# Kernel optimization log

Hardware: AMD Instinct MI355X
Metric: run time of the kernel (lower is better)

The kernel has to match this reference:

```python
import jax, jax.numpy as jnp
import numpy as np

H = 8          # num_heads
D = 64         # head_dim
HID = 512      # hidden_size
W = 128        # window_size
NEG = -1e9

def setup_inputs() -> dict:
    key = jax.random.key(0)
    ks = jax.random.split(key, 12)
    B, S = 2, 2048
    def lin(i):
        w = jax.random.normal(ks[i], (HID, HID), dtype=jnp.float32) * (1.0 / np.sqrt(HID))
        b = jax.random.normal(ks[i + 1], (HID,), dtype=jnp.float32) * 0.01
        return w, b
    Wq, bq = lin(0)
    Wk, bk = lin(2)
    Wv, bv = lin(4)
    Wo, bo = lin(6)
    return {
        "value": jax.random.normal(ks[8], (B, S, HID), dtype=jnp.float32),
        "key": jax.random.normal(ks[9], (B, S, HID), dtype=jnp.float32),
        "query": jax.random.normal(ks[10], (B, S, HID), dtype=jnp.float32),
        "Wq": Wq, "bq": bq, "Wk": Wk, "bk": bk,
        "Wv": Wv, "bv": bv, "Wo": Wo, "bo": bo,
    }

def reference(value, key, query, Wq, bq, Wk, bk, Wv, bv, Wo, bo):
    B, S, _ = query.shape
    def heads(x, Wt, b):
        # torch Linear: x @ W.T + b ; then [B,S,H,D] -> [B,H,S,D]
        return (x @ Wt.T + b).reshape(B, S, H, D).transpose(0, 2, 1, 3)
    Q = heads(query, Wq, bq)
    K = heads(key, Wk, bk)
    V = heads(value, Wv, bv)
    scores = jnp.einsum('bhqd,bhkd->bhqk', Q, K) / jnp.sqrt(jnp.float32(D))
    idx = jnp.arange(S)
    local = jnp.abs(idx[:, None] - idx[None, :]) <= W  # [S,S] band mask
    scores = jnp.where(local[None, None], scores, NEG)
    weights = jax.nn.softmax(scores, axis=-1)
    out = jnp.einsum('bhqk,bhkd->bhqd', weights, V)
    out = out.transpose(0, 2, 1, 3).reshape(B, S, HID)
    return out @ Wo.T + bo
```

## Files before the change

kernel.cpp:

```cpp
#include <hip/hip_runtime.h>
#include <stdint.h>

#define B_   2
#define S_   2048
#define H_   8
#define D_   64
#define HID_ 512
#define W_   128
#define M_   (B_ * S_)
#define E_   (M_ * HID_)
#define PPAD_ 72
#define M0_  12.0f

typedef unsigned short u16;
typedef __attribute__((ext_vector_type(8))) __bf16 bf16x8;
typedef __attribute__((ext_vector_type(4))) float  floatx4;

__device__ __forceinline__ float b2f(u16 u) {
    union { unsigned int i; float f; } x;
    x.i = ((unsigned int)u) << 16;
    return x.f;
}
__device__ __forceinline__ u16 f2b(float f) {
    union { float f; unsigned int i; } x;
    x.f = f;
    unsigned int r = x.i + 0x7FFFu + ((x.i >> 16) & 1u);
    return (u16)(r >> 16);
}

__device__ __forceinline__ void gll16(const u16* g, u16* l) {
    __builtin_amdgcn_global_load_lds(
        (const __attribute__((address_space(1))) unsigned int*)g,
        (__attribute__((address_space(3))) unsigned int*)l, 16, 0, 0);
}

__device__ __forceinline__ void cvt8_store(float4 a, float4 b, u16* dst) {
    bf16x8 v;
    v[0] = (__bf16)a.x; v[1] = (__bf16)a.y; v[2] = (__bf16)a.z; v[3] = (__bf16)a.w;
    v[4] = (__bf16)b.x; v[5] = (__bf16)b.y; v[6] = (__bf16)b.z; v[7] = (__bf16)b.w;
    *(bf16x8*)dst = v;
}

template <int MODE>
__device__ __forceinline__ void gemm_fp32in_body(
    const float* __restrict__ Xf, const float* __restrict__ Wf,
    const float* __restrict__ bias, u16* __restrict__ outH) {
    __shared__ u16 As[128 * 32];
    __shared__ u16 Bs[64 * 32];

    const int tid  = threadIdx.x;
    const int wave = tid >> 6;
    const int lane = tid & 63;
    const int r16  = lane & 15;
    const int quad = lane >> 4;
    const int m0 = blockIdx.x * 128;
    const int n0 = blockIdx.y * 64;
    const int m_base = m0 + wave * 64;

    const int ar = tid >> 2;
    const int ak = (tid & 3) * 8;
    const int br = tid >> 1;
    const int bk2 = (tid & 1) * 16;

    floatx4 zero = {0.f, 0.f, 0.f, 0.f};
    floatx4 acc[4][4];
#pragma unroll
    for (int i = 0; i < 4; i++)
#pragma unroll
        for (int j = 0; j < 4; j++) acc[i][j] = zero;

    for (int k0 = 0; k0 < HID_; k0 += 32) {
        __syncthreads();
#pragma unroll
        for (int e = 0; e < 4; e++) {
            const int row = e * 32 + ar;
            const float4* src = (const float4*)(Xf + (size_t)(m0 + row) * HID_ + k0 + ak);
            cvt8_store(src[0], src[1], &As[row * 32 + ak]);
        }
        {
            const float4* src = (const float4*)(Wf + (size_t)(n0 + br) * HID_ + k0 + bk2);
            cvt8_store(src[0], src[1], &Bs[br * 32 + bk2]);
            cvt8_store(src[2], src[3], &Bs[br * 32 + bk2 + 8]);
        }
        __syncthreads();

        bf16x8 a0[4], b[4];
#pragma unroll
        for (int t = 0; t < 4; t++) {
            a0[t] = *(const bf16x8*)&As[(wave * 64 + t * 16 + r16) * 32 + quad * 8];
            b[t]  = *(const bf16x8*)&Bs[(t * 16 + r16) * 32 + quad * 8];
        }
#pragma unroll
        for (int i = 0; i < 4; i++)
#pragma unroll
            for (int j = 0; j < 4; j++)
                acc[i][j] = __builtin_amdgcn_mfma_f32_16x16x32_bf16(a0[i], b[j], acc[i][j], 0, 0, 0);
    }

    const int bb = m_base >> 11;
    if (MODE == 1) {
#pragma unroll
        for (int j = 0; j < 4; j++) {
            const int col = n0 + j * 16 + r16;
            const int h = col >> 6, d = col & (D_ - 1);
            const float bv = bias[col];
            const size_t base = (size_t)(bb * H_ + h) * S_;
#pragma unroll
            for (int i = 0; i < 4; i++)
#pragma unroll
                for (int r = 0; r < 4; r++) {
                    const int s = (m_base & (S_ - 1)) + i * 16 + quad * 4 + r;
                    outH[(base + s) * D_ + d] = f2b(acc[i][j][r] + bv);
                }
        }
    } else {
#pragma unroll
        for (int j = 0; j < 4; j++) {
            const int col = n0 + j * 16 + r16;
            const int h = col >> 6, d = col & (D_ - 1);
            const float bv = bias[col];
            const size_t base = ((size_t)(bb * H_ + h) * D_ + d) * S_;
            const int s0 = (m_base & (S_ - 1)) + quad * 4;
#pragma unroll
            for (int i = 0; i < 4; i++) {
                ushort4 hs;
                hs.x = f2b(acc[i][j][0] + bv);
                hs.y = f2b(acc[i][j][1] + bv);
                hs.z = f2b(acc[i][j][2] + bv);
                hs.w = f2b(acc[i][j][3] + bv);
                *(ushort4*)(outH + base + s0 + i * 16) = hs;
            }
        }
    }
}

__global__ __launch_bounds__(128) void qkv_fused_kernel(
    const float* __restrict__ xq, const float* __restrict__ xk, const float* __restrict__ xv,
    const float* __restrict__ wq, const float* __restrict__ wk, const float* __restrict__ wv,
    const float* __restrict__ bq, const float* __restrict__ bk, const float* __restrict__ bv,
    u16* __restrict__ P) {
    if (blockIdx.z == 0)      gemm_fp32in_body<1>(xq, wq, bq, P);
    else if (blockIdx.z == 1) gemm_fp32in_body<1>(xk, wk, bk, P + E_);
    else                      gemm_fp32in_body<2>(xv, wv, bv, P + 2 * (size_t)E_);
}

__global__ __launch_bounds__(128) void out_fused_kernel(
    const u16* __restrict__ AOh, const float* __restrict__ Wf,
    const float* __restrict__ bias, float* __restrict__ outF) {
    __shared__ u16 As[128 * 32];
    __shared__ u16 Bs[64 * 32];

    const int tid  = threadIdx.x;
    const int wave = tid >> 6;
    const int lane = tid & 63;
    const int r16  = lane & 15;
    const int quad = lane >> 4;
    const int lrow = lane >> 2;
    const int lk   = (lane & 3) * 8;
    const int br   = tid >> 1;
    const int bk2  = (tid & 1) * 16;
    const int m0 = blockIdx.x * 128;
    const int n0 = blockIdx.y * 64;
    const int m_base = m0 + wave * 64;

    floatx4 zero = {0.f, 0.f, 0.f, 0.f};
    floatx4 acc[4][4];
#pragma unroll
    for (int i = 0; i < 4; i++)
#pragma unroll
        for (int j = 0; j < 4; j++) acc[i][j] = zero;

    for (int k0 = 0; k0 < HID_; k0 += 32) {
        __syncthreads();
#pragma unroll
        for (int e = 0; e < 4; e++) {
            const int row = wave * 64 + e * 16 + lrow;
            gll16(AOh + (size_t)(m0 + row) * HID_ + k0 + lk,
                  &As[(wave * 64 + e * 16) * 32]);
        }
        {
            const float4* src = (const float4*)(Wf + (size_t)(n0 + br) * HID_ + k0 + bk2);
            cvt8_store(src[0], src[1], &Bs[br * 32 + bk2]);
            cvt8_store(src[2], src[3], &Bs[br * 32 + bk2 + 8]);
        }
        __syncthreads();

        bf16x8 a0[4], b[4];
#pragma unroll
        for (int t = 0; t < 4; t++) {
            a0[t] = *(const bf16x8*)&As[(wave * 64 + t * 16 + r16) * 32 + quad * 8];
            b[t]  = *(const bf16x8*)&Bs[(t * 16 + r16) * 32 + quad * 8];
        }
#pragma unroll
        for (int i = 0; i < 4; i++)
#pragma unroll
            for (int j = 0; j < 4; j++)
                acc[i][j] = __builtin_amdgcn_mfma_f32_16x16x32_bf16(a0[i], b[j], acc[i][j], 0, 0, 0);
    }

#pragma unroll
    for (int j = 0; j < 4; j++) {
        const int col = n0 + j * 16 + r16;
        const float bv = bias[col];
#pragma unroll
        for (int i = 0; i < 4; i++) {
            const int row0 = m_base + i * 16 + quad * 4;
#pragma unroll
            for (int r = 0; r < 4; r++)
                outF[(size_t)(row0 + r) * HID_ + col] = acc[i][j][r] + bv;
        }
    }
}

__global__ __launch_bounds__(256) void attn_kernel(
    const u16* __restrict__ Qh, const u16* __restrict__ Kh,
    const u16* __restrict__ Vth, u16* __restrict__ AOh) {
    __shared__ u16   Ps[4][64][PPAD_];
    __shared__ float Ored[64][68];
    __shared__ float Lred[4][64];

    const int tid  = threadIdx.x;
    const int wave = tid >> 6;
    const int lane = tid & 63;
    const int r16 = lane & 15, quad = lane >> 4;
    const int qt = blockIdx.x, bh = blockIdx.y;
    const int q0 = qt * 64;
    const size_t sd = (size_t)bh * S_ * D_;
    const size_t ds = (size_t)bh * D_ * S_;

    floatx4 zero = {0.f, 0.f, 0.f, 0.f};
    floatx4 O[4][4];
    float lsum[4][4];
#pragma unroll
    for (int i = 0; i < 4; i++)
#pragma unroll
        for (int j = 0; j < 4; j++) O[i][j] = zero;
#pragma unroll
    for (int i = 0; i < 4; i++)
#pragma unroll
        for (int r = 0; r < 4; r++) lsum[i][r] = 0.f;

    int t_lo = qt - 2; if (t_lo < 0) t_lo = 0;
    int t_hi = qt + 2; if (t_hi > S_ / 64 - 1) t_hi = S_ / 64 - 1;

    for (int t = t_lo + wave; t <= t_hi; t += 4) {
        const int k0 = t * 64;
        floatx4 sa[4][4];
#pragma unroll
        for (int i = 0; i < 4; i++)
#pragma unroll
            for (int j = 0; j < 4; j++) sa[i][j] = zero;

#pragma unroll
        for (int ks = 0; ks < 2; ks++) {
            bf16x8 qf[4], kf[4];
#pragma unroll
            for (int i = 0; i < 4; i++)
                qf[i] = *(const bf16x8*)(Qh + sd + (size_t)(q0 + i * 16 + r16) * D_ + ks * 32 + quad * 8);
#pragma unroll
            for (int j = 0; j < 4; j++)
                kf[j] = *(const bf16x8*)(Kh + sd + (size_t)(k0 + j * 16 + r16) * D_ + ks * 32 + quad * 8);
#pragma unroll
            for (int i = 0; i < 4; i++)
#pragma unroll
                for (int j = 0; j < 4; j++)
                    sa[i][j] = __builtin_amdgcn_mfma_f32_16x16x32_bf16(qf[i], kf[j], sa[i][j], 0, 0, 0);
        }

#pragma unroll
        for (int i = 0; i < 4; i++)
#pragma unroll
            for (int j = 0; j < 4; j++) {
                const int kc = k0 + j * 16 + r16;
#pragma unroll
                for (int r = 0; r < 4; r++) {
                    const int q = q0 + i * 16 + quad * 4 + r;
                    const bool valid = (unsigned)(kc - q + W_) <= (unsigned)(2 * W_);
                    const float p = valid ? __expf(fmaf(sa[i][j][r], 0.125f, -M0_)) : 0.f;
                    lsum[i][r] += p;
                    Ps[wave][i * 16 + quad * 4 + r][j * 16 + r16] = f2b(p);
                }
            }

#pragma unroll
        for (int ks = 0; ks < 2; ks++) {
            bf16x8 pf[4], vf[4];
#pragma unroll
            for (int i = 0; i < 4; i++)
                pf[i] = *(const bf16x8*)&Ps[wave][i * 16 + r16][ks * 32 + quad * 8];
#pragma unroll
            for (int j = 0; j < 4; j++)
                vf[j] = *(const bf16x8*)(Vth + ds + (size_t)(j * 16 + r16) * S_ + k0 + ks * 32 + quad * 8);
#pragma unroll
            for (int i = 0; i < 4; i++)
#pragma unroll
                for (int j = 0; j < 4; j++)
                    O[i][j] = __builtin_amdgcn_mfma_f32_16x16x32_bf16(pf[i], vf[j], O[i][j], 0, 0, 0);
        }
    }

#pragma unroll
    for (int i = 0; i < 4; i++)
#pragma unroll
        for (int r = 0; r < 4; r++) {
            float l = lsum[i][r];
#pragma unroll
            for (int off = 1; off < 16; off <<= 1) l += __shfl_xor(l, off, 64);
            if (r16 == 0) Lred[wave][i * 16 + quad * 4 + r] = l;
        }

    const bool active = (t_lo + wave <= t_hi);
#pragma unroll
    for (int w = 0; w < 4; w++) {
        if (wave == w && active) {
#pragma unroll
            for (int i = 0; i < 4; i++)
#pragma unroll
                for (int j = 0; j < 4; j++) {
                    floatx4* cell = (floatx4*)&Ored[j * 16 + r16][i * 16 + quad * 4];
                    if (w == 0) *cell = O[i][j];
                    else        *cell = *cell + O[i][j];
                }
        }
        __syncthreads();
    }

    const int b = bh >> 3, h = bh & 7;
    const int q  = tid >> 2;
    const int d0 = (tid & 3) * 16;
    const float linv = 1.f / (Lred[0][q] + Lred[1][q] + Lred[2][q] + Lred[3][q]);
    const size_t base = (size_t)(b * S_ + q0 + q) * HID_ + h * D_ + d0;
#pragma unroll
    for (int k = 0; k < 16; k++)
        AOh[base + k] = f2b(Ored[d0 + k][q] * linv);
}

extern "C" void kernel_launch(void* const* d_in, const int* in_sizes, int n_in,
                              void* d_out, int out_size, void* d_ws, size_t ws_size,
                              hipStream_t stream) {
    const float* value = (const float*)d_in[0];
    const float* key_  = (const float*)d_in[1];
    const float* query = (const float*)d_in[2];
    const float* Wq = (const float*)d_in[3];
    const float* bq = (const float*)d_in[4];
    const float* Wk = (const float*)d_in[5];
    const float* bk = (const float*)d_in[6];
    const float* Wv = (const float*)d_in[7];
    const float* bv = (const float*)d_in[8];
    const float* Wo = (const float*)d_in[9];
    const float* bo = (const float*)d_in[10];

    u16* P   = (u16*)d_ws;
    u16* AOh = P + 3 * (size_t)E_;

    qkv_fused_kernel<<<dim3(M_ / 128, HID_ / 64, 3), 128, 0, stream>>>(
        query, key_, value, Wq, Wk, Wv, bq, bk, bv, P);
    attn_kernel<<<dim3(S_ / 64, B_ * H_), 256, 0, stream>>>(
        P, P + E_, P + 2 * (size_t)E_, AOh);
    out_fused_kernel<<<dim3(M_ / 128, HID_ / 64), 128, 0, stream>>>(
        AOh, Wo, bo, (float*)d_out);
}
```

Baseline: 148.7 us.

## Double-buffer GEMM tiles and repartition attention waves by query rows

Both projection GEMMs now use double-buffered LDS with register prefetch of the next K-tile, so global loads overlap the MFMA work on the current tile. The output GEMM also drops the direct global-to-LDS loads in favour of the same register-staged path. The attention kernel gives each wave its own 16 query rows and has it loop over every key tile, instead of splitting key tiles across waves. That removes the cross-wave LDS reduction, the block barriers and the Lred buffer, and lets each wave write its output as vectorized stores. In exchange each wave does more serial key tiles, more register state is held for prefetch, and K/V fragments are reloaded per wave.

Measured after the change: 143.2 us. 1.04x faster.

```diff
diff --git a/kernel.cpp b/kernel.cpp
--- a/kernel.cpp
+++ b/kernel.cpp
@@ -16,11 +16,6 @@
 typedef __attribute__((ext_vector_type(8))) __bf16 bf16x8;
 typedef __attribute__((ext_vector_type(4))) float  floatx4;
 
-__device__ __forceinline__ float b2f(u16 u) {
-    union { unsigned int i; float f; } x;
-    x.i = ((unsigned int)u) << 16;
-    return x.f;
-}
 __device__ __forceinline__ u16 f2b(float f) {
     union { float f; unsigned int i; } x;
     x.f = f;
@@ -28,12 +23,6 @@
     return (u16)(r >> 16);
 }
 
-__device__ __forceinline__ void gll16(const u16* g, u16* l) {
-    __builtin_amdgcn_global_load_lds(
-        (const __attribute__((address_space(1))) unsigned int*)g,
-        (__attribute__((address_space(3))) unsigned int*)l, 16, 0, 0);
-}
-
 __device__ __forceinline__ void cvt8_store(float4 a, float4 b, u16* dst) {
     bf16x8 v;
     v[0] = (__bf16)a.x; v[1] = (__bf16)a.y; v[2] = (__bf16)a.z; v[3] = (__bf16)a.w;
@@ -41,12 +30,28 @@
     *(bf16x8*)dst = v;
 }
 
+__device__ __forceinline__ void mfma_tile(const u16* As, const u16* Bs,
+                                          int wave, int r16, int quad,
+                                          floatx4 acc[4][4]) {
+    bf16x8 a0[4], b[4];
+#pragma unroll
+    for (int t = 0; t < 4; t++) {
+        a0[t] = *(const bf16x8*)&As[(wave * 64 + t * 16 + r16) * 32 + quad * 8];
+        b[t]  = *(const bf16x8*)&Bs[(t * 16 + r16) * 32 + quad * 8];
+    }
+#pragma unroll
+    for (int i = 0; i < 4; i++)
+#pragma unroll
+        for (int j = 0; j < 4; j++)
+            acc[i][j] = __builtin_amdgcn_mfma_f32_16x16x32_bf16(a0[i], b[j], acc[i][j], 0, 0, 0);
+}
+
 template <int MODE>
 __device__ __forceinline__ void gemm_fp32in_body(
     const float* __restrict__ Xf, const float* __restrict__ Wf,
     const float* __restrict__ bias, u16* __restrict__ outH) {
-    __shared__ u16 As[128 * 32];
-    __shared__ u16 Bs[64 * 32];
+    __shared__ u16 As[2][128 * 32];
+    __shared__ u16 Bs[2][64 * 32];
 
     const int tid  = threadIdx.x;
     const int wave = tid >> 6;
@@ -57,9 +62,9 @@
     const int n0 = blockIdx.y * 64;
     const int m_base = m0 + wave * 64;
 
-    const int ar = tid >> 2;
-    const int ak = (tid & 3) * 8;
-    const int br = tid >> 1;
+    const int ar  = tid >> 2;
+    const int ak  = (tid & 3) * 8;
+    const int br  = tid >> 1;
     const int bk2 = (tid & 1) * 16;
 
     floatx4 zero = {0.f, 0.f, 0.f, 0.f};
@@ -69,33 +74,42 @@
 #pragma unroll
         for (int j = 0; j < 4; j++) acc[i][j] = zero;
 
-    for (int k0 = 0; k0 < HID_; k0 += 32) {
+    float4 rA0[8], rB0[4], rA1[8], rB1[4];
+
+#define LOADT(rA, rB, k0) do {                                                 \
+        _Pragma("unroll")                                                      \
+        for (int e = 0; e < 4; e++) {                                          \
+            const float4* s_ = (const float4*)(Xf + (size_t)(m0 + e * 32 + ar) * HID_ + (k0) + ak); \
+            rA[2 * e] = s_[0]; rA[2 * e + 1] = s_[1];                          \
+        }                                                                      \
+        const float4* w_ = (const float4*)(Wf + (size_t)(n0 + br) * HID_ + (k0) + bk2); \
+        rB[0] = w_[0]; rB[1] = w_[1]; rB[2] = w_[2]; rB[3] = w_[3];            \
+    } while (0)
+#define STORET(rA, rB, buf) do {                                               \
+        _Pragma("unroll")                                                      \
+        for (int e = 0; e < 4; e++)                                            \
+            cvt8_store(rA[2 * e], rA[2 * e + 1], &As[buf][(e * 32 + ar) * 32 + ak]); \
+        cvt8_store(rB[0], rB[1], &Bs[buf][br * 32 + bk2]);                     \
+        cvt8_store(rB[2], rB[3], &Bs[buf][br * 32 + bk2 + 8]);                 \
+    } while (0)
+
+    LOADT(rA0, rB0, 0);
+    LOADT(rA1, rB1, 32);
+    STORET(rA0, rB0, 0);
+    __syncthreads();
+
+    for (int t = 0; t < 16; t += 2) {
+        if (t + 2 < 16) LOADT(rA0, rB0, (t + 2) * 32);
+        mfma_tile(As[0], Bs[0], wave, r16, quad, acc);
+        STORET(rA1, rB1, 1);
         __syncthreads();
-#pragma unroll
-        for (int e = 0; e < 4; e++) {
-            const int row = e * 32 + ar;
-            const float4* src = (const float4*)(Xf + (size_t)(m0 + row) * HID_ + k0 + ak);
-            cvt8_store(src[0], src[1], &As[row * 32 + ak]);
-        }
-        {
-            const float4* src = (const float4*)(Wf + (size_t)(n0 + br) * HID_ + k0 + bk2);
-            cvt8_store(src[0], src[1], &Bs[br * 32 + bk2]);
-            cvt8_store(src[2], src[3], &Bs[br * 32 + bk2 + 8]);
-        }
+        if (t + 3 < 16) LOADT(rA1, rB1, (t + 3) * 32);
+        mfma_tile(As[1], Bs[1], wave, r16, quad, acc);
+        if (t + 2 < 16) STORET(rA0, rB0, 0);
         __syncthreads();
-
-        bf16x8 a0[4], b[4];
-#pragma unroll
-        for (int t = 0; t < 4; t++) {
-            a0[t] = *(const bf16x8*)&As[(wave * 64 + t * 16 + r16) * 32 + quad * 8];
-            b[t]  = *(const bf16x8*)&Bs[(t * 16 + r16) * 32 + quad * 8];
-        }
-#pragma unroll
-        for (int i = 0; i < 4; i++)
-#pragma unroll
-            for (int j = 0; j < 4; j++)
-                acc[i][j] = __builtin_amdgcn_mfma_f32_16x16x32_bf16(a0[i], b[j], acc[i][j], 0, 0, 0);
-    }
+    }
+#undef LOADT
+#undef STORET
 
     const int bb = m_base >> 11;
     if (MODE == 1) {
@@ -147,22 +161,23 @@
 __global__ __launch_bounds__(128) void out_fused_kernel(
     const u16* __restrict__ AOh, const float* __restrict__ Wf,
     const float* __restrict__ bias, float* __restrict__ outF) {
-    __shared__ u16 As[128 * 32];
-    __shared__ u16 Bs[64 * 32];
+    __shared__ u16 As[2][128 * 32];
+    __shared__ u16 Bs[2][64 * 32];
 
     const int tid  = threadIdx.x;
     const int wave = tid >> 6;
     const int lane = tid & 63;
     const int r16  = lane & 15;
     const int quad = lane >> 4;
-    const int lrow = lane >> 2;
-    const int lk   = (lane & 3) * 8;
-    const int br   = tid >> 1;
-    const int bk2  = (tid & 1) * 16;
     const int m0 = blockIdx.x * 128;
     const int n0 = blockIdx.y * 64;
     const int m_base = m0 + wave * 64;
 
+    const int ar  = tid >> 2;
+    const int ak  = (tid & 3) * 8;
+    const int br  = tid >> 1;
+    const int bk2 = (tid & 1) * 16;
+
     floatx4 zero = {0.f, 0.f, 0.f, 0.f};
     floatx4 acc[4][4];
 #pragma unroll
@@ -170,33 +185,41 @@
 #pragma unroll
         for (int j = 0; j < 4; j++) acc[i][j] = zero;
 
-    for (int k0 = 0; k0 < HID_; k0 += 32) {
+    uint4  rA0[4], rA1[4];
+    float4 rB0[4], rB1[4];
+
+#define LOADO(rA, rB, k0) do {                                                 \
+        _Pragma("unroll")                                                      \
+        for (int e = 0; e < 4; e++)                                            \
+            rA[e] = *(const uint4*)(AOh + (size_t)(m0 + e * 32 + ar) * HID_ + (k0) + ak); \
+        const float4* w_ = (const float4*)(Wf + (size_t)(n0 + br) * HID_ + (k0) + bk2); \
+        rB[0] = w_[0]; rB[1] = w_[1]; rB[2] = w_[2]; rB[3] = w_[3];            \
+    } while (0)
+#define STOREO(rA, rB, buf) do {                                               \
+        _Pragma("unroll")                                                      \
+        for (int e = 0; e < 4; e++)                                            \
+            *(uint4*)&As[buf][(e * 32 + ar) * 32 + ak] = rA[e];                \
+        cvt8_store(rB[0], rB[1], &Bs[buf][br * 32 + bk2]);                     \
+        cvt8_store(rB[2], rB[3], &Bs[buf][br * 32 + bk2 + 8]);                 \
+    } while (0)
+
+    LOADO(rA0, rB0, 0);
+    LOADO(rA1, rB1, 32);
+    STOREO(rA0, rB0, 0);
+    __syncthreads();
+
+    for (int t = 0; t < 16; t += 2) {
+        if (t + 2 < 16) LOADO(rA0, rB0, (t + 2) * 32);
+        mfma_tile(As[0], Bs[0], wave, r16, quad, acc);
+        STOREO(rA1, rB1, 1);
         __syncthreads();
-#pragma unroll
-        for (int e = 0; e < 4; e++) {
-            const int row = wave * 64 + e * 16 + lrow;
-            gll16(AOh + (size_t)(m0 + row) * HID_ + k0 + lk,
-                  &As[(wave * 64 + e * 16) * 32]);
-        }
-        {
-            const float4* src = (const float4*)(Wf + (size_t)(n0 + br) * HID_ + k0 + bk2);
-            cvt8_store(src[0], src[1], &Bs[br * 32 + bk2]);
-            cvt8_store(src[2], src[3], &Bs[br * 32 + bk2 + 8]);
-        }
+        if (t + 3 < 16) LOADO(rA1, rB1, (t + 3) * 32);
+        mfma_tile(As[1], Bs[1], wave, r16, quad, acc);
+        if (t + 2 < 16) STOREO(rA0, rB0, 0);
         __syncthreads();
-
-        bf16x8 a0[4], b[4];
-#pragma unroll
-        for (int t = 0; t < 4; t++) {
-            a0[t] = *(const bf16x8*)&As[(wave * 64 + t * 16 + r16) * 32 + quad * 8];
-            b[t]  = *(const bf16x8*)&Bs[(t * 16 + r16) * 32 + quad * 8];
-        }
-#pragma unroll
-        for (int i = 0; i < 4; i++)
-#pragma unroll
-            for (int j = 0; j < 4; j++)
-                acc[i][j] = __builtin_amdgcn_mfma_f32_16x16x32_bf16(a0[i], b[j], acc[i][j], 0, 0, 0);
-    }
+    }
+#undef LOADO
+#undef STOREO
 
 #pragma unroll
     for (int j = 0; j < 4; j++) {
@@ -215,124 +238,97 @@
 __global__ __launch_bounds__(256) void attn_kernel(
     const u16* __restrict__ Qh, const u16* __restrict__ Kh,
     const u16* __restrict__ Vth, u16* __restrict__ AOh) {
-    __shared__ u16   Ps[4][64][PPAD_];
-    __shared__ float Ored[64][68];
-    __shared__ float Lred[4][64];
+    __shared__ u16 Ps[4][16][PPAD_];
+    __shared__ u16 Osh[4][16][PPAD_];
 
     const int tid  = threadIdx.x;
     const int wave = tid >> 6;
     const int lane = tid & 63;
     const int r16 = lane & 15, quad = lane >> 4;
     const int qt = blockIdx.x, bh = blockIdx.y;
-    const int q0 = qt * 64;
+    const int q0 = qt * 64 + wave * 16;
     const size_t sd = (size_t)bh * S_ * D_;
     const size_t ds = (size_t)bh * D_ * S_;
 
+    bf16x8 qf[2];
+#pragma unroll
+    for (int ks = 0; ks < 2; ks++)
+        qf[ks] = *(const bf16x8*)(Qh + sd + (size_t)(q0 + r16) * D_ + ks * 32 + quad * 8);
+
     floatx4 zero = {0.f, 0.f, 0.f, 0.f};
-    floatx4 O[4][4];
-    float lsum[4][4];
-#pragma unroll
-    for (int i = 0; i < 4; i++)
-#pragma unroll
-        for (int j = 0; j < 4; j++) O[i][j] = zero;
-#pragma unroll
-    for (int i = 0; i < 4; i++)
-#pragma unroll
-        for (int r = 0; r < 4; r++) lsum[i][r] = 0.f;
+    floatx4 O[4];
+    float lsum[4];
+#pragma unroll
+    for (int j = 0; j < 4; j++) O[j] = zero;
+#pragma unroll
+    for (int r = 0; r < 4; r++) lsum[r] = 0.f;
 
     int t_lo = qt - 2; if (t_lo < 0) t_lo = 0;
     int t_hi = qt + 2; if (t_hi > S_ / 64 - 1) t_hi = S_ / 64 - 1;
 
-    for (int t = t_lo + wave; t <= t_hi; t += 4) {
+    for (int t = t_lo; t <= t_hi; ++t) {
         const int k0 = t * 64;
-        floatx4 sa[4][4];
-#pragma unroll
-        for (int i = 0; i < 4; i++)
-#pragma unroll
-            for (int j = 0; j < 4; j++) sa[i][j] = zero;
+        floatx4 sa[4];
+#pragma unroll
+        for (int j = 0; j < 4; j++) sa[j] = zero;
 
 #pragma unroll
         for (int ks = 0; ks < 2; ks++) {
-            bf16x8 qf[4], kf[4];
-#pragma unroll
-            for (int i = 0; i < 4; i++)
-                qf[i] = *(const bf16x8*)(Qh + sd + (size_t)(q0 + i * 16 + r16) * D_ + ks * 32 + quad * 8);
+            bf16x8 kf[4];
 #pragma unroll
             for (int j = 0; j < 4; j++)
                 kf[j] = *(const bf16x8*)(Kh + sd + (size_t)(k0 + j * 16 + r16) * D_ + ks * 32 + quad * 8);
 #pragma unroll
-            for (int i = 0; i < 4; i++)
-#pragma unroll
-                for (int j = 0; j < 4; j++)
-                    sa[i][j] = __builtin_amdgcn_mfma_f32_16x16x32_bf16(qf[i], kf[j], sa[i][j], 0, 0, 0);
-        }
-
-#pragma unroll
-        for (int i = 0; i < 4; i++)
+            for (int j = 0; j < 4; j++)
+                sa[j] = __builtin_amdgcn_mfma_f32_16x16x32_bf16(qf[ks], kf[j], sa[j], 0, 0, 0);
+        }
+
+#pragma unroll
+        for (int j = 0; j < 4; j++) {
+            const int kc = k0 + j * 16 + r16;
+#pragma unroll
+            for (int r = 0; r < 4; r++) {
+                const int q = q0 + quad * 4 + r;
+                const bool valid = (unsigned)(kc - q + W_) <= (unsigned)(2 * W_);
+                const float p = valid ? __expf(fmaf(sa[j][r], 0.125f, -M0_)) : 0.f;
+                lsum[r] += p;
+                Ps[wave][quad * 4 + r][j * 16 + r16] = f2b(p);
+            }
+        }
+
+#pragma unroll
+        for (int ks = 0; ks < 2; ks++) {
+            bf16x8 pf = *(const bf16x8*)&Ps[wave][r16][ks * 32 + quad * 8];
 #pragma unroll
             for (int j = 0; j < 4; j++) {
-                const int kc = k0 + j * 16 + r16;
-#pragma unroll
-                for (int r = 0; r < 4; r++) {
-                    const int q = q0 + i * 16 + quad * 4 + r;
-                    const bool valid = (unsigned)(kc - q + W_) <= (unsigned)(2 * W_);
-                    const float p = valid ? __expf(fmaf(sa[i][j][r], 0.125f, -M0_)) : 0.f;
-                    lsum[i][r] += p;
-                    Ps[wave][i * 16 + quad * 4 + r][j * 16 + r16] = f2b(p);
-                }
+                bf16x8 vf = *(const bf16x8*)(Vth + ds + (size_t)(j * 16 + r16) * S_ + k0 + ks * 32 + quad * 8);
+                O[j] = __builtin_amdgcn_mfma_f32_16x16x32_bf16(pf, vf, O[j], 0, 0, 0);
             }
-
-#pragma unroll
-        for (int ks = 0; ks < 2; ks++) {
-            bf16x8 pf[4], vf[4];
-#pragma unroll
-            for (int i = 0; i < 4; i++)
-                pf[i] = *(const bf16x8*)&Ps[wave][i * 16 + r16][ks * 32 + quad * 8];
-#pragma unroll
-            for (int j = 0; j < 4; j++)
-                vf[j] = *(const bf16x8*)(Vth + ds + (size_t)(j * 16 + r16) * S_ + k0 + ks * 32 + quad * 8);
-#pragma unroll
-            for (int i = 0; i < 4; i++)
-#pragma unroll
-                for (int j = 0; j < 4; j++)
-                    O[i][j] = __builtin_amdgcn_mfma_f32_16x16x32_bf16(pf[i], vf[j], O[i][j], 0, 0, 0);
-        }
-    }
-
-#pragma unroll
-    for (int i = 0; i < 4; i++)
-#pragma unroll
-        for (int r = 0; r < 4; r++) {
-            float l = lsum[i][r];
-#pragma unroll
-            for (int off = 1; off < 16; off <<= 1) l += __shfl_xor(l, off, 64);
-            if (r16 == 0) Lred[wave][i * 16 + quad * 4 + r] = l;
-        }
-
-    const bool active = (t_lo + wave <= t_hi);
-#pragma unroll
-    for (int w = 0; w < 4; w++) {
-        if (wave == w && active) {
-#pragma unroll
-            for (int i = 0; i < 4; i++)
-#pragma unroll
-                for (int j = 0; j < 4; j++) {
-                    floatx4* cell = (floatx4*)&Ored[j * 16 + r16][i * 16 + quad * 4];
-                    if (w == 0) *cell = O[i][j];
-                    else        *cell = *cell + O[i][j];
-                }
-        }
-        __syncthreads();
+        }
+    }
+
+#pragma unroll
+    for (int r = 0; r < 4; r++) {
+        float l = lsum[r];
+#pragma unroll
+        for (int off = 1; off < 16; off <<= 1) l += __shfl_xor(l, off, 64);
+        lsum[r] = l;
+    }
+
+#pragma unroll
+    for (int r = 0; r < 4; r++) {
+        const float linv = 1.f / lsum[r];
+#pragma unroll
+        for (int j = 0; j < 4; j++)
+            Osh[wave][quad * 4 + r][j * 16 + r16] = f2b(O[j][r] * linv);
     }
 
     const int b = bh >> 3, h = bh & 7;
-    const int q  = tid >> 2;
-    const int d0 = (tid & 3) * 16;
-    const float linv = 1.f / (Lred[0][q] + Lred[1][q] + Lred[2][q] + Lred[3][q]);
-    const size_t base = (size_t)(b * S_ + q0 + q) * HID_ + h * D_ + d0;
-#pragma unroll
-    for (int k = 0; k < 16; k++)
-        AOh[base + k] = f2b(Ored[d0 + k][q] * linv);
+    const int qq = lane >> 2;
+    const int d0 = (lane & 3) * 16;
+    u16* dst = AOh + (size_t)(b * S_ + q0 + qq) * HID_ + h * D_ + d0;
+    *(uint4*)dst       = *(const uint4*)&Osh[wave][qq][d0];
+    *(uint4*)(dst + 8) = *(const uint4*)&Osh[wave][qq][d0 + 8];
 }
 
 extern "C" void kernel_launch(void* const* d_in, const int* in_sizes, int n_in,
```
